# Kernel optimization log

Measured on AMD Instinct MI355X. Metric: run time of the kernel, lower is better.

The kernel has to match this reference:

```python
import jax, jax.numpy as jnp
import numpy as np

MUL = 128   # multiplicity of every l in the input/output irreps
C   = 128   # channel count of the grid signal
LIN = 3     # lmax of irreps_in / irreps_out
LV  = 2     # VSH lmax = lmax - 1
NB  = 8     # res_beta  = 2*(lmax+1)
NA  = 7     # res_alpha = 2*lmax + 1
NLM = (LV + 1) ** 2  # 9 spherical-harmonic coefficients per component


def _sh_basis(L, Nb, Na):
    """Real orthonormal spherical harmonics on a Gauss-Legendre x uniform-alpha grid.
    Returns Y [(L+1)^2, Nb, Na] and quadrature weights qw [Nb, Na] so that
    sum_grid Y_i * Y_j * qw = delta_ij (exact at these resolutions)."""
    x, w = np.polynomial.legendre.leggauss(Nb)        # cos(beta) nodes/weights
    s = np.sqrt(1.0 - x * x)                          # sin(beta)
    alpha = 2.0 * np.pi * np.arange(Na) / Na
    # normalized associated Legendre Pbar[l, m, beta]
    P = np.zeros((L + 1, L + 1, Nb))
    P[0, 0] = np.sqrt(1.0 / (4.0 * np.pi))
    for m in range(1, L + 1):
        P[m, m] = -np.sqrt((2.0 * m + 1.0) / (2.0 * m)) * s * P[m - 1, m - 1]
    for m in range(0, L):
        P[m + 1, m] = np.sqrt(2.0 * m + 3.0) * x * P[m, m]
    for m in range(0, L + 1):
        for l in range(m + 2, L + 1):
            a = np.sqrt((4.0 * l * l - 1.0) / (l * l - m * m))
            b = np.sqrt(((l - 1.0) ** 2 - m * m) / (4.0 * (l - 1.0) ** 2 - 1.0))
            P[l, m] = a * (x * P[l - 1, m] - b * P[l - 2, m])
    Y = np.zeros(((L + 1) ** 2, Nb, Na))
    idx = 0
    for l in range(L + 1):
        for m in range(-l, l + 1):
            if m == 0:
                Y[idx] = P[l, 0][:, None] * np.ones(Na)[None, :]
            elif m > 0:
                Y[idx] = np.sqrt(2.0) * P[l, m][:, None] * np.cos(m * alpha)[None, :]
            else:
                Y[idx] = np.sqrt(2.0) * P[l, -m][:, None] * np.sin(-m * alpha)[None, :]
            idx += 1
    qw = (w[:, None] * (2.0 * np.pi / Na)) * np.ones(Na)[None, :]
    return Y.astype(np.float32), qw.astype(np.float32)


_Y_NP, _QW_NP = _sh_basis(LV, NB, NA)
_YJ = jnp.asarray(_Y_NP)              # [9, NB, NA]  synthesis basis
_YW = jnp.asarray(_Y_NP * _QW_NP)     # [9, NB, NA]  analysis (quadrature-weighted) basis


def _irreps_to_vsh_coeffs(x, W):
    """e3nn-style per-l Linear from input irreps (mul=MUL, l=0..LIN) to VSH coeffs.
    x: [B, MUL*sum(2l+1)], W: [LV+1, MUL, C, 4]. Input l-blocks above LV have no
    matching output irrep and are dropped (as e3nn Linear would).
    Returns [B, C, 4, NLM]."""
    coeffs, off = [], 0
    for l in range(LIN + 1):
        d = 2 * l + 1
        blk = x[:, off:off + MUL * d].reshape(-1, MUL, d)
        off += MUL * d
        if l <= LV:
            coeffs.append(jnp.einsum('bum,ucp->bcpm', blk, W[l]) / np.sqrt(MUL))
    return jnp.concatenate(coeffs, axis=-1)


def setup_inputs() -> dict:
    key = jax.random.key(0)
    k1, k2, k3, k4, k5 = jax.random.split(key, 5)
    B = 2048
    IN_DIM = MUL * sum(2 * l + 1 for l in range(LIN + 1))  # 2048
    return {
        'x1':   jax.random.normal(k1, (B, IN_DIM), dtype=jnp.float32),
        'x2':   jax.random.normal(k2, (B, IN_DIM), dtype=jnp.float32),
        'W1':   jax.random.normal(k3, (LV + 1, MUL, C, 4), dtype=jnp.float32),
        'W2':   jax.random.normal(k4, (LV + 1, MUL, C, 4), dtype=jnp.float32),
        'Wout': jax.random.normal(k5, (LV + 1, C, 4, MUL), dtype=jnp.float32),
    }


def reference(x1, x2, W1, W2, Wout):
    B = x1.shape[0]
    # equivariant linears -> VSH coefficients  [B, C, 4, 9]
    c1 = _irreps_to_vsh_coeffs(x1, W1)
    c2 = _irreps_to_vsh_coeffs(x2, W2)
    # to_vector_signal: SH synthesis per component -> [B, C, 4, NB, NA]
    s1 = jnp.einsum('bcpk,kxy->bcpxy', c1, _YJ)
    s2 = jnp.einsum('bcpk,kxy->bcpxy', c2, _YJ)
    # per-grid-point product: scalar mul on component 0, cross product on 1:4
    out_sig = jnp.concatenate(
        [s1[:, :, :1] * s2[:, :, :1],
         jnp.cross(s1[:, :, 1:], s2[:, :, 1:], axis=2)], axis=2)
    # from_vector_signal: quadrature SH analysis -> [B, C, 4, 9]
    c_out = jnp.einsum('bcpxy,kxy->bcpk', out_sig, _YW)
    # final equivariant linear back to output irreps (l<=LV paths; l=3 block has
    # no path from the VSH irreps so it is zero, matching e3nn Linear)
    blocks = []
    for l in range(LV + 1):
        d = 2 * l + 1
        cl = c_out[..., l * l:(l + 1) ** 2]                       # [B, C, 4, d]
        blk = jnp.einsum('bcpm,cpu->bum', cl, Wout[l]) / np.sqrt(4 * C)
        blocks.append(blk.reshape(B, MUL * d))
    blocks.append(jnp.zeros((B, MUL * (2 * LIN + 1)), dtype=x1.dtype))
    return jnp.concatenate(blocks, axis=-1)
```

## Files before the change

### kernel.cpp

```cpp
#include <hip/hip_runtime.h>
#include <math.h>

typedef short short8 __attribute__((ext_vector_type(8)));
typedef float f32x4 __attribute__((ext_vector_type(4)));

#define B_N 2048
#define NKM 9
#define CP 512
#define KU 128
#define STG 132
#define INV_SQRT_MUL 0.08838834764831845f
#define INV_SQRT_4C  0.04419417382415922f

__device__ ushort g_xb1[NKM * B_N * KU];
__device__ ushort g_xb2[NKM * B_N * KU];
__device__ ushort g_W1bt[3 * CP * KU];
__device__ ushort g_W2bt[3 * CP * KU];
__device__ ushort g_Woutbt[3 * KU * CP];
__device__ ushort g_cb[(size_t)B_N * NKM * CP];

__device__ __forceinline__ ushort f2b(float f) {
    uint u = __float_as_uint(f);
    uint r = (u + 0x7fffu + ((u >> 16) & 1u)) >> 16;
    return (ushort)r;
}
__device__ __forceinline__ float pk_lo(uint u) { return __uint_as_float(u << 16); }
__device__ __forceinline__ float pk_hi(uint u) { return __uint_as_float(u & 0xffff0000u); }
__device__ __forceinline__ int l_of_km(int km) { return (km >= 4) ? 2 : (km >= 1 ? 1 : 0); }

__host__ __device__ constexpr int lof(int n) { return n >= 4 ? 2 : (n >= 1 ? 1 : 0); }
__host__ __device__ constexpr int mof(int n) { int l = lof(n); return n - l * l - l; }
__host__ __device__ constexpr bool gaunt_nz(int a, int b, int c) {
    int la = lof(a), lb = lof(b), lc = lof(c);
    if ((la + lb + lc) & 1) return false;
    if (lc > la + lb || la > lb + lc || lb > lc + la) return false;
    int ma = mof(a), mb = mof(b), mc = mof(c);
    int neg = (ma < 0) + (mb < 0) + (mc < 0);
    if (neg & 1) return false;
    int A = ma < 0 ? -ma : ma, Bm = mb < 0 ? -mb : mb, Cm = mc < 0 ? -mc : mc;
    return (A + Bm == Cm) || (Bm + Cm == A) || (Cm + A == Bm);
}
__host__ __device__ constexpr float gaunt_val(int a, int b, int c) {
    int x = a, y = b, z = c, t = 0;
    if (x > y) { t = x; x = y; y = t; }
    if (y > z) { t = y; y = z; z = t; }
    if (x > y) { t = x; x = y; y = t; }
    const float C00 = 0.28209479177387814f;
    const float A_  = 0.12615662610100802f;
    const float B_  = 0.25231325220201604f;
    const float C_  = 0.21850968611841584f;
    const float D_  = 0.18022375157286857f;
    const float E_  = 0.09011187578643429f;
    const float F_  = 0.15607834722743988f;
    if (x == 0) return C00;
    if (y <= 3) {
        if (z == 6) return (y == 2) ? B_ : -A_;
        if (z == 8) return (x == 1) ? -C_ : C_;
        return C_;
    }
    if (x == 4) return (y == 4) ? -D_ : F_;
    if (x == 5) return (z == 6) ? E_ : -F_;
    if (x == 6) return (y == 6) ? D_ : ((y == 7) ? E_ : -D_);
    return F_;
}
struct IEnt { int k, j; float v; };
struct ITab { IEnt e[16]; int n; };
__host__ __device__ constexpr ITab make_it(int ii) {
    ITab t{};
    for (int k = 0; k < 9; ++k)
        for (int j = 0; j < 9; ++j)
            if (gaunt_nz(k, ii, j)) {
                t.e[t.n].k = k; t.e[t.n].j = j; t.e[t.n].v = gaunt_val(k, ii, j);
                ++t.n;
            }
    return t;
}

template <int I>
__device__ __forceinline__ void mid_step(const ushort* __restrict__ c1s,
                                         int mb, int mc,
                                         const float (&f2v)[2][9][4],
                                         float (&o)[2][4][9]) {
    constexpr ITab T = make_it(I);
    #pragma unroll
    for (int un = 0; un < 2; ++un) {
        int cc = mc + un * 16;
        uint2 v = *(const uint2*)&c1s[mb * STG + cc * 4];
        float a0 = pk_lo(v.x), a1 = pk_hi(v.x);
        float a2 = pk_lo(v.y), a3 = pk_hi(v.y);
        #pragma unroll
        for (int e = 0; e < T.n; ++e) {
            const int   k = T.e[e].k, j = T.e[e].j;
            const float g = T.e[e].v;
            float d0 = f2v[un][j][0], d1 = f2v[un][j][1];
            float d2 = f2v[un][j][2], d3 = f2v[un][j][3];
            o[un][0][k] = fmaf(g, a0 * d0, o[un][0][k]);
            o[un][1][k] = fmaf(g, fmaf(a2, d3, -(a3 * d2)), o[un][1][k]);
            o[un][2][k] = fmaf(g, fmaf(a3, d1, -(a1 * d3)), o[un][2][k]);
            o[un][3][k] = fmaf(g, fmaf(a1, d2, -(a2 * d1)), o[un][3][k]);
        }
    }
}

__global__ __launch_bounds__(256) void prep_kernel(const float* __restrict__ x1,
                                                   const float* __restrict__ x2,
                                                   const float* __restrict__ W1,
                                                   const float* __restrict__ W2,
                                                   const float* __restrict__ Wout,
                                                   float* __restrict__ out) {
    int bid = blockIdx.x, tid = threadIdx.x;
    if (bid >= B_N) {
        int idx = (bid - B_N) * 256 + tid;
        int l = idx >> 16;
        int r = idx & 65535;
        {
            int cp = r >> 7, u = r & 127;
            size_t src = (size_t)l * 65536 + (size_t)u * 512 + cp;
            g_W1bt[idx] = f2b(W1[src] * INV_SQRT_MUL);
            g_W2bt[idx] = f2b(W2[src] * INV_SQRT_MUL);
        }
        {
            int u = r >> 9, cp = r & 511;
            g_Woutbt[idx] = f2b(Wout[(size_t)l * 65536 + (size_t)cp * 128 + u] * INV_SQRT_4C);
        }
        return;
    }
    int b = bid;
    __shared__ float L1[2048], L2[2048];
    const float4* r1 = (const float4*)(x1 + (size_t)b * 2048);
    const float4* r2 = (const float4*)(x2 + (size_t)b * 2048);
    #pragma unroll
    for (int i = 0; i < 2; ++i) {
        int q = i * 256 + tid;
        *(float4*)&L1[q * 4] = r1[q];
        *(float4*)&L2[q * 4] = r2[q];
    }
    float4 z = make_float4(0.f, 0.f, 0.f, 0.f);
    if (tid < 224) *(float4*)&out[(size_t)b * 2048 + 1152 + tid * 4] = z;
    __syncthreads();
    #pragma unroll
    for (int i = 0; i < 9; ++i) {
        int e = i * 256 + tid;
        int field = e >= 1152;
        int r = e - field * 1152;
        int km = r >> 7, u = r & 127;
        int l = l_of_km(km);
        int col = l * l * 128 + u * (2 * l + 1) + (km - l * l);
        float v = field ? L2[col] : L1[col];
        ushort* dst = field ? g_xb2 : g_xb1;
        dst[(size_t)km * (B_N * KU) + (size_t)b * KU + u] = f2b(v);
    }
}

__device__ __forceinline__ void load_A16(const ushort* __restrict__ xa, int b0,
                                         int tid, ushort* As) {
    int row = tid >> 4, kg = tid & 15;
    int dst = row * 128 + ((kg ^ (row & 7)) << 3);
    *(short8*)&As[dst] = *(const short8*)&xa[(size_t)(b0 + row) * KU + (kg << 3)];
}
__device__ __forceinline__ void load_B128(const ushort* __restrict__ wb, int n0,
                                          int tid, ushort* Bs) {
    #pragma unroll
    for (int it = 0; it < 8; ++it) {
        int i = it * 256 + tid;
        int row = i >> 4, kg = i & 15;
        int dst = row * 128 + ((kg ^ (row & 7)) << 3);
        *(short8*)&Bs[dst] = *(const short8*)&wb[(size_t)(n0 + row) * KU + (kg << 3)];
    }
}
__device__ __forceinline__ void gemm16x128(const ushort* As, const ushort* Bs,
                                           int lane, int wid, ushort* stage) {
    f32x4 acc0 = (f32x4){0.f, 0.f, 0.f, 0.f};
    f32x4 acc1 = (f32x4){0.f, 0.f, 0.f, 0.f};
    #pragma unroll
    for (int ks = 0; ks < 4; ++ks) {
        int kg = ks * 4 + (lane >> 4);
        int ar = lane & 15;
        short8 a = *(const short8*)&As[ar * 128 + ((kg ^ (ar & 7)) << 3)];
        int br0 = wid * 32 + (lane & 15);
        short8 b0v = *(const short8*)&Bs[br0 * 128 + ((kg ^ (br0 & 7)) << 3)];
        acc0 = __builtin_amdgcn_mfma_f32_16x16x32_bf16(a, b0v, acc0, 0, 0, 0);
        int br1 = br0 + 16;
        short8 b1v = *(const short8*)&Bs[br1 * 128 + ((kg ^ (br1 & 7)) << 3)];
        acc1 = __builtin_amdgcn_mfma_f32_16x16x32_bf16(a, b1v, acc1, 0, 0, 0);
    }
    #pragma unroll
    for (int r = 0; r < 4; ++r) {
        int row = ((lane >> 4) << 2) + r;
        stage[row * STG + wid * 32 + (lane & 15)]      = f2b(acc0[r]);
        stage[row * STG + wid * 32 + 16 + (lane & 15)] = f2b(acc1[r]);
    }
}

__global__ __launch_bounds__(256) void cmid_kernel() {
    __shared__ ushort As[16 * 128];
    __shared__ ushort Bs[128 * 128];
    __shared__ ushort c1s[16 * STG];
    __shared__ ushort c2s[9][16 * STG];

    int tid = threadIdx.x;
    int n0 = blockIdx.x * 128, b0 = blockIdx.y * 16;
    int lane = tid & 63, wid = tid >> 6;
    int mb = tid >> 4, mc = tid & 15;

#define F2_STEP(KM) \
    load_A16(g_xb2 + (size_t)(KM) * (B_N * KU), b0, tid, As); \
    __syncthreads(); \
    gemm16x128(As, Bs, lane, wid, &c2s[KM][0]); \
    __syncthreads();

    load_B128(g_W2bt + 0 * 65536, n0, tid, Bs);
    F2_STEP(0)
    load_B128(g_W2bt + 1 * 65536, n0, tid, Bs);
    F2_STEP(1) F2_STEP(2) F2_STEP(3)
    load_B128(g_W2bt + 2 * 65536, n0, tid, Bs);
    F2_STEP(4) F2_STEP(5) F2_STEP(6) F2_STEP(7) F2_STEP(8)
#undef F2_STEP

    float f2v[2][9][4];
    #pragma unroll
    for (int k = 0; k < 9; ++k) {
        #pragma unroll
        for (int un = 0; un < 2; ++un) {
            int cc = mc + un * 16;
            uint2 v = *(const uint2*)&c2s[k][mb * STG + cc * 4];
            f2v[un][k][0] = pk_lo(v.x); f2v[un][k][1] = pk_hi(v.x);
            f2v[un][k][2] = pk_lo(v.y); f2v[un][k][3] = pk_hi(v.y);
        }
    }

    float o[2][4][9];
    #pragma unroll
    for (int un = 0; un < 2; ++un)
        #pragma unroll
        for (int p = 0; p < 4; ++p)
            #pragma unroll
            for (int k = 0; k < 9; ++k) o[un][p][k] = 0.f;

#define F1_STEP(KM) \
    load_A16(g_xb1 + (size_t)(KM) * (B_N * KU), b0, tid, As); \
    __syncthreads(); \
    gemm16x128(As, Bs, lane, wid, c1s); \
    __syncthreads(); \
    mid_step<KM>(c1s, mb, mc, f2v, o);

    load_B128(g_W1bt + 0 * 65536, n0, tid, Bs);
    F1_STEP(0)
    load_B128(g_W1bt + 1 * 65536, n0, tid, Bs);
    F1_STEP(1) F1_STEP(2) F1_STEP(3)
    load_B128(g_W1bt + 2 * 65536, n0, tid, Bs);
    F1_STEP(4) F1_STEP(5) F1_STEP(6) F1_STEP(7) F1_STEP(8)
#undef F1_STEP

    #pragma unroll
    for (int un = 0; un < 2; ++un) {
        int cc = mc + un * 16;
        ushort* w = g_cb + (size_t)(b0 + mb) * (NKM * CP) + n0 + cc * 4;
        #pragma unroll
        for (int k = 0; k < 9; ++k) {
            uint2 st;
            st.x = (uint)f2b(o[un][0][k]) | ((uint)f2b(o[un][1][k]) << 16);
            st.y = (uint)f2b(o[un][2][k]) | ((uint)f2b(o[un][3][k]) << 16);
            *(uint2*)&w[(size_t)k * CP] = st;
        }
    }
}

__global__ __launch_bounds__(256) void out_gemm_kernel(float* __restrict__ out) {
    __shared__ ushort Aso[64 * 128];
    __shared__ ushort Bso[128 * 128];
    int tid = threadIdx.x;
    int km = blockIdx.y;
    int l = l_of_km(km);
    int mi = km - l * l, d = 2 * l + 1, OFF = 128 * l * l;
    int b0 = blockIdx.x * 64;

    int lane = tid & 63, wid = tid >> 6, wr = wid >> 1, wc = wid & 1;
    f32x4 acc[2][4];
    #pragma unroll
    for (int i = 0; i < 2; ++i)
        #pragma unroll
        for (int j = 0; j < 4; ++j) acc[i][j] = (f32x4){0.f, 0.f, 0.f, 0.f};

    for (int kc = 0; kc < 4; ++kc) {
        #pragma unroll
        for (int it = 0; it < 4; ++it) {
            int i = it * 256 + tid;
            int row = i >> 4, kg = i & 15;
            int dst = row * 128 + ((kg ^ (row & 7)) << 3);
            *(short8*)&Aso[dst] = *(const short8*)&g_cb[(size_t)(b0 + row) * (NKM * CP)
                                                       + (size_t)km * CP + kc * 128 + (kg << 3)];
        }
        #pragma unroll
        for (int it = 0; it < 8; ++it) {
            int i = it * 256 + tid;
            int row = i >> 4, kg = i & 15;
            int dst = row * 128 + ((kg ^ (row & 7)) << 3);
            *(short8*)&Bso[dst] = *(const short8*)&g_Woutbt[(size_t)l * 65536
                                                       + (size_t)row * CP + kc * 128 + (kg << 3)];
        }
        __syncthreads();
        #pragma unroll
        for (int ks = 0; ks < 4; ++ks) {
            int kg = ks * 4 + (lane >> 4);
            short8 a[2], b[4];
            #pragma unroll
            for (int i = 0; i < 2; ++i) {
                int row = wr * 32 + i * 16 + (lane & 15);
                a[i] = *(const short8*)&Aso[row * 128 + ((kg ^ (row & 7)) << 3)];
            }
            #pragma unroll
            for (int j = 0; j < 4; ++j) {
                int row = wc * 64 + j * 16 + (lane & 15);
                b[j] = *(const short8*)&Bso[row * 128 + ((kg ^ (row & 7)) << 3)];
            }
            #pragma unroll
            for (int i = 0; i < 2; ++i)
                #pragma unroll
                for (int j = 0; j < 4; ++j)
                    acc[i][j] = __builtin_amdgcn_mfma_f32_16x16x32_bf16(a[i], b[j], acc[i][j], 0, 0, 0);
        }
        __syncthreads();
    }

    #pragma unroll
    for (int i = 0; i < 2; ++i)
        #pragma unroll
        for (int j = 0; j < 4; ++j)
            #pragma unroll
            for (int r = 0; r < 4; ++r) {
                int row = b0 + wr * 32 + i * 16 + ((lane >> 4) << 2) + r;
                int u   = wc * 64 + j * 16 + (lane & 15);
                out[(size_t)row * 2048 + OFF + u * d + mi] = acc[i][j][r];
            }
}

extern "C" void kernel_launch(void* const* d_in, const int* in_sizes, int n_in,
                              void* d_out, int out_size, void* d_ws, size_t ws_size,
                              hipStream_t stream) {
    const float* x1   = (const float*)d_in[0];
    const float* x2   = (const float*)d_in[1];
    const float* W1   = (const float*)d_in[2];
    const float* W2   = (const float*)d_in[3];
    const float* Wout = (const float*)d_in[4];
    float* out = (float*)d_out;

    prep_kernel<<<B_N + 768, 256, 0, stream>>>(x1, x2, W1, W2, Wout, out);
    cmid_kernel<<<dim3(4, B_N / 16), 256, 0, stream>>>();
    out_gemm_kernel<<<dim3(B_N / 64, NKM), 256, 0, stream>>>(out);
}
```

Before: 64.84 us.

## Halve cmid column tile and double-buffer A loads across unified 18-step schedule

The cmid kernel now processes 64 output columns per block instead of 128, which doubles the grid and shrinks per-thread registers (f2v/o arrays halved) and shared memory (c2s staging array removed). The 18 GEMM steps (9 for field 2, 9 for field 1) are unrolled through a templated step that prefetches the next A tile into a second shared buffer while the current MFMA runs, and reloads B only when the l-block changes. The intent is higher occupancy and overlap of global loads with compute. The cost is that every W tile and every x row tile is now fetched by twice as many blocks.

```diff
diff --git a/kernel.cpp b/kernel.cpp
--- a/kernel.cpp
+++ b/kernel.cpp
@@ -8,7 +8,7 @@
 #define NKM 9
 #define CP 512
 #define KU 128
-#define STG 132
+#define STG 68
 #define INV_SQRT_MUL 0.08838834764831845f
 #define INV_SQRT_4C  0.04419417382415922f
 
@@ -79,26 +79,22 @@
 template <int I>
 __device__ __forceinline__ void mid_step(const ushort* __restrict__ c1s,
                                          int mb, int mc,
-                                         const float (&f2v)[2][9][4],
-                                         float (&o)[2][4][9]) {
+                                         const float (&f2v)[9][4],
+                                         float (&o)[4][9]) {
     constexpr ITab T = make_it(I);
-    #pragma unroll
-    for (int un = 0; un < 2; ++un) {
-        int cc = mc + un * 16;
-        uint2 v = *(const uint2*)&c1s[mb * STG + cc * 4];
-        float a0 = pk_lo(v.x), a1 = pk_hi(v.x);
-        float a2 = pk_lo(v.y), a3 = pk_hi(v.y);
-        #pragma unroll
-        for (int e = 0; e < T.n; ++e) {
-            const int   k = T.e[e].k, j = T.e[e].j;
-            const float g = T.e[e].v;
-            float d0 = f2v[un][j][0], d1 = f2v[un][j][1];
-            float d2 = f2v[un][j][2], d3 = f2v[un][j][3];
-            o[un][0][k] = fmaf(g, a0 * d0, o[un][0][k]);
-            o[un][1][k] = fmaf(g, fmaf(a2, d3, -(a3 * d2)), o[un][1][k]);
-            o[un][2][k] = fmaf(g, fmaf(a3, d1, -(a1 * d3)), o[un][2][k]);
-            o[un][3][k] = fmaf(g, fmaf(a1, d2, -(a2 * d1)), o[un][3][k]);
-        }
+    uint2 v = *(const uint2*)&c1s[mb * STG + mc * 4];
+    float a0 = pk_lo(v.x), a1 = pk_hi(v.x);
+    float a2 = pk_lo(v.y), a3 = pk_hi(v.y);
+    #pragma unroll
+    for (int e = 0; e < T.n; ++e) {
+        const int   k = T.e[e].k, j = T.e[e].j;
+        const float g = T.e[e].v;
+        float d0 = f2v[j][0], d1 = f2v[j][1];
+        float d2 = f2v[j][2], d3 = f2v[j][3];
+        o[0][k] = fmaf(g, a0 * d0, o[0][k]);
+        o[1][k] = fmaf(g, fmaf(a2, d3, -(a3 * d2)), o[1][k]);
+        o[2][k] = fmaf(g, fmaf(a3, d1, -(a1 * d3)), o[2][k]);
+        o[3][k] = fmaf(g, fmaf(a1, d2, -(a2 * d1)), o[3][k]);
     }
 }
 
@@ -152,117 +148,129 @@
     }
 }
 
-__device__ __forceinline__ void load_A16(const ushort* __restrict__ xa, int b0,
-                                         int tid, ushort* As) {
-    int row = tid >> 4, kg = tid & 15;
-    int dst = row * 128 + ((kg ^ (row & 7)) << 3);
-    *(short8*)&As[dst] = *(const short8*)&xa[(size_t)(b0 + row) * KU + (kg << 3)];
-}
-__device__ __forceinline__ void load_B128(const ushort* __restrict__ wb, int n0,
-                                          int tid, ushort* Bs) {
-    #pragma unroll
-    for (int it = 0; it < 8; ++it) {
+__device__ __forceinline__ void load_B64(const ushort* __restrict__ wb, int n0,
+                                         int tid, ushort* Bs) {
+    #pragma unroll
+    for (int it = 0; it < 4; ++it) {
         int i = it * 256 + tid;
         int row = i >> 4, kg = i & 15;
         int dst = row * 128 + ((kg ^ (row & 7)) << 3);
         *(short8*)&Bs[dst] = *(const short8*)&wb[(size_t)(n0 + row) * KU + (kg << 3)];
     }
 }
-__device__ __forceinline__ void gemm16x128(const ushort* As, const ushort* Bs,
-                                           int lane, int wid, ushort* stage) {
-    f32x4 acc0 = (f32x4){0.f, 0.f, 0.f, 0.f};
-    f32x4 acc1 = (f32x4){0.f, 0.f, 0.f, 0.f};
+__device__ __forceinline__ void gemm16x64(const ushort* As_, const ushort* Bs_,
+                                          int lane, int wid, ushort* stage) {
+    f32x4 acc = (f32x4){0.f, 0.f, 0.f, 0.f};
     #pragma unroll
     for (int ks = 0; ks < 4; ++ks) {
         int kg = ks * 4 + (lane >> 4);
         int ar = lane & 15;
-        short8 a = *(const short8*)&As[ar * 128 + ((kg ^ (ar & 7)) << 3)];
-        int br0 = wid * 32 + (lane & 15);
-        short8 b0v = *(const short8*)&Bs[br0 * 128 + ((kg ^ (br0 & 7)) << 3)];
-        acc0 = __builtin_amdgcn_mfma_f32_16x16x32_bf16(a, b0v, acc0, 0, 0, 0);
-        int br1 = br0 + 16;
-        short8 b1v = *(const short8*)&Bs[br1 * 128 + ((kg ^ (br1 & 7)) << 3)];
-        acc1 = __builtin_amdgcn_mfma_f32_16x16x32_bf16(a, b1v, acc1, 0, 0, 0);
+        short8 a = *(const short8*)&As_[ar * 128 + ((kg ^ (ar & 7)) << 3)];
+        int br = wid * 16 + (lane & 15);
+        short8 b = *(const short8*)&Bs_[br * 128 + ((kg ^ (br & 7)) << 3)];
+        acc = __builtin_amdgcn_mfma_f32_16x16x32_bf16(a, b, acc, 0, 0, 0);
     }
     #pragma unroll
     for (int r = 0; r < 4; ++r) {
         int row = ((lane >> 4) << 2) + r;
-        stage[row * STG + wid * 32 + (lane & 15)]      = f2b(acc0[r]);
-        stage[row * STG + wid * 32 + 16 + (lane & 15)] = f2b(acc1[r]);
+        stage[row * STG + wid * 16 + (lane & 15)] = f2b(acc[r]);
+    }
+}
+
+template <int S>
+__device__ __forceinline__ void cmid_step(int b0, int n0, int tid, int lane, int wid,
+                                          int mb, int mc,
+                                          ushort* As0, ushort* As1,
+                                          ushort* Bs, ushort* stage,
+                                          float (&f2v)[9][4], float (&o)[4][9]) {
+    constexpr int fld  = (S < 9) ? 2 : 1;
+    constexpr int km   = S % 9;
+    constexpr bool hasNext = (S < 17);
+    constexpr int Sn   = hasNext ? S + 1 : S;
+    constexpr int nfld = (Sn < 9) ? 2 : 1;
+    constexpr int nkm  = Sn % 9;
+    constexpr int nl   = (nkm >= 4) ? 2 : (nkm >= 1 ? 1 : 0);
+    constexpr int cl   = (km  >= 4) ? 2 : (km  >= 1 ? 1 : 0);
+    constexpr bool newB = hasNext && (nl != cl || nfld != fld);
+
+    ushort* Acur = (S & 1) ? As1 : As0;
+    ushort* Anxt = (S & 1) ? As0 : As1;
+
+    __syncthreads();
+    int arow = tid >> 4, akg = tid & 15;
+    short8 av;
+    if constexpr (hasNext) {
+        const ushort* xsrc = (nfld == 2 ? g_xb2 : g_xb1) + (size_t)nkm * (B_N * KU);
+        av = *(const short8*)&xsrc[(size_t)(b0 + arow) * KU + (akg << 3)];
+    }
+    gemm16x64(Acur, Bs, lane, wid, stage);
+    __syncthreads();
+    if constexpr (hasNext)
+        *(short8*)&Anxt[arow * 128 + ((akg ^ (arow & 7)) << 3)] = av;
+    if constexpr (fld == 2) {
+        uint2 v = *(const uint2*)&stage[mb * STG + mc * 4];
+        f2v[km][0] = pk_lo(v.x); f2v[km][1] = pk_hi(v.x);
+        f2v[km][2] = pk_lo(v.y); f2v[km][3] = pk_hi(v.y);
+    } else {
+        mid_step<km>(stage, mb, mc, f2v, o);
+    }
+    if constexpr (newB) {
+        const ushort* wsrc = (nfld == 2 ? g_W2bt : g_W1bt) + (size_t)nl * 65536;
+        load_B64(wsrc, n0, tid, Bs);
     }
 }
 
 __global__ __launch_bounds__(256) void cmid_kernel() {
-    __shared__ ushort As[16 * 128];
-    __shared__ ushort Bs[128 * 128];
-    __shared__ ushort c1s[16 * STG];
-    __shared__ ushort c2s[9][16 * STG];
+    __shared__ ushort As0[16 * 128];
+    __shared__ ushort As1[16 * 128];
+    __shared__ ushort Bs[64 * 128];
+    __shared__ ushort stage[16 * STG];
 
     int tid = threadIdx.x;
-    int n0 = blockIdx.x * 128, b0 = blockIdx.y * 16;
+    int n0 = blockIdx.x * 64, b0 = blockIdx.y * 16;
     int lane = tid & 63, wid = tid >> 6;
     int mb = tid >> 4, mc = tid & 15;
 
-#define F2_STEP(KM) \
-    load_A16(g_xb2 + (size_t)(KM) * (B_N * KU), b0, tid, As); \
-    __syncthreads(); \
-    gemm16x128(As, Bs, lane, wid, &c2s[KM][0]); \
-    __syncthreads();
-
-    load_B128(g_W2bt + 0 * 65536, n0, tid, Bs);
-    F2_STEP(0)
-    load_B128(g_W2bt + 1 * 65536, n0, tid, Bs);
-    F2_STEP(1) F2_STEP(2) F2_STEP(3)
-    load_B128(g_W2bt + 2 * 65536, n0, tid, Bs);
-    F2_STEP(4) F2_STEP(5) F2_STEP(6) F2_STEP(7) F2_STEP(8)
-#undef F2_STEP
-
-    float f2v[2][9][4];
+    load_B64(g_W2bt, n0, tid, Bs);
+    {
+        int arow = tid >> 4, akg = tid & 15;
+        *(short8*)&As0[arow * 128 + ((akg ^ (arow & 7)) << 3)] =
+            *(const short8*)&g_xb2[(size_t)(b0 + arow) * KU + (akg << 3)];
+    }
+
+    float f2v[9][4];
+    float o[4][9];
+    #pragma unroll
+    for (int p = 0; p < 4; ++p)
+        #pragma unroll
+        for (int k = 0; k < 9; ++k) o[p][k] = 0.f;
+
+    cmid_step<0>(b0, n0, tid, lane, wid, mb, mc, As0, As1, Bs, stage, f2v, o);
+    cmid_step<1>(b0, n0, tid, lane, wid, mb, mc, As0, As1, Bs, stage, f2v, o);
+    cmid_step<2>(b0, n0, tid, lane, wid, mb, mc, As0, As1, Bs, stage, f2v, o);
+    cmid_step<3>(b0, n0, tid, lane, wid, mb, mc, As0, As1, Bs, stage, f2v, o);
+    cmid_step<4>(b0, n0, tid, lane, wid, mb, mc, As0, As1, Bs, stage, f2v, o);
+    cmid_step<5>(b0, n0, tid, lane, wid, mb, mc, As0, As1, Bs, stage, f2v, o);
+    cmid_step<6>(b0, n0, tid, lane, wid, mb, mc, As0, As1, Bs, stage, f2v, o);
+    cmid_step<7>(b0, n0, tid, lane, wid, mb, mc, As0, As1, Bs, stage, f2v, o);
+    cmid_step<8>(b0, n0, tid, lane, wid, mb, mc, As0, As1, Bs, stage, f2v, o);
+    cmid_step<9>(b0, n0, tid, lane, wid, mb, mc, As0, As1, Bs, stage, f2v, o);
+    cmid_step<10>(b0, n0, tid, lane, wid, mb, mc, As0, As1, Bs, stage, f2v, o);
+    cmid_step<11>(b0, n0, tid, lane, wid, mb, mc, As0, As1, Bs, stage, f2v, o);
+    cmid_step<12>(b0, n0, tid, lane, wid, mb, mc, As0, As1, Bs, stage, f2v, o);
+    cmid_step<13>(b0, n0, tid, lane, wid, mb, mc, As0, As1, Bs, stage, f2v, o);
+    cmid_step<14>(b0, n0, tid, lane, wid, mb, mc, As0, As1, Bs, stage, f2v, o);
+    cmid_step<15>(b0, n0, tid, lane, wid, mb, mc, As0, As1, Bs, stage, f2v, o);
+    cmid_step<16>(b0, n0, tid, lane, wid, mb, mc, As0, As1, Bs, stage, f2v, o);
+    cmid_step<17>(b0, n0, tid, lane, wid, mb, mc, As0, As1, Bs, stage, f2v, o);
+
+    ushort* w = g_cb + (size_t)(b0 + mb) * (NKM * CP) + n0 + mc * 4;
     #pragma unroll
     for (int k = 0; k < 9; ++k) {
-        #pragma unroll
-        for (int un = 0; un < 2; ++un) {
-            int cc = mc + un * 16;
-            uint2 v = *(const uint2*)&c2s[k][mb * STG + cc * 4];
-            f2v[un][k][0] = pk_lo(v.x); f2v[un][k][1] = pk_hi(v.x);
-            f2v[un][k][2] = pk_lo(v.y); f2v[un][k][3] = pk_hi(v.y);
-        }
-    }
-
-    float o[2][4][9];
-    #pragma unroll
-    for (int un = 0; un < 2; ++un)
-        #pragma unroll
-        for (int p = 0; p < 4; ++p)
-            #pragma unroll
-            for (int k = 0; k < 9; ++k) o[un][p][k] = 0.f;
-
-#define F1_STEP(KM) \
-    load_A16(g_xb1 + (size_t)(KM) * (B_N * KU), b0, tid, As); \
-    __syncthreads(); \
-    gemm16x128(As, Bs, lane, wid, c1s); \
-    __syncthreads(); \
-    mid_step<KM>(c1s, mb, mc, f2v, o);
-
-    load_B128(g_W1bt + 0 * 65536, n0, tid, Bs);
-    F1_STEP(0)
-    load_B128(g_W1bt + 1 * 65536, n0, tid, Bs);
-    F1_STEP(1) F1_STEP(2) F1_STEP(3)
-    load_B128(g_W1bt + 2 * 65536, n0, tid, Bs);
-    F1_STEP(4) F1_STEP(5) F1_STEP(6) F1_STEP(7) F1_STEP(8)
-#undef F1_STEP
-
-    #pragma unroll
-    for (int un = 0; un < 2; ++un) {
-        int cc = mc + un * 16;
-        ushort* w = g_cb + (size_t)(b0 + mb) * (NKM * CP) + n0 + cc * 4;
-        #pragma unroll
-        for (int k = 0; k < 9; ++k) {
-            uint2 st;
-            st.x = (uint)f2b(o[un][0][k]) | ((uint)f2b(o[un][1][k]) << 16);
-            st.y = (uint)f2b(o[un][2][k]) | ((uint)f2b(o[un][3][k]) << 16);
-            *(uint2*)&w[(size_t)k * CP] = st;
-        }
+        uint2 st;
+        st.x = (uint)f2b(o[0][k]) | ((uint)f2b(o[1][k]) << 16);
+        st.y = (uint)f2b(o[2][k]) | ((uint)f2b(o[3][k]) << 16);
+        *(uint2*)&w[(size_t)k * CP] = st;
     }
 }
 
@@ -346,6 +354,6 @@
     float* out = (float*)d_out;
 
     prep_kernel<<<B_N + 768, 256, 0, stream>>>(x1, x2, W1, W2, Wout, out);
-    cmid_kernel<<<dim3(4, B_N / 16), 256, 0, stream>>>();
+    cmid_kernel<<<dim3(CP / 64, B_N / 16), 256, 0, stream>>>();
     out_gemm_kernel<<<dim3(B_N / 64, NKM), 256, 0, stream>>>(out);
 }
```

After: 69.26 us. +6.8%, slower.
